# Performance work log

Measured on AMD Instinct MI355X. Metric: run time of the kernel, lower is better.

## Reference

```python
import jax, jax.numpy as jnp
from jax import lax
import numpy as np


def _conv(x, w):
    # x: [B,Cin,H,W], w: [Cout,Cin,kh,kw] -> [B,Cout,H,W], SAME padding
    return lax.conv_general_dilated(x, w, (1, 1), 'SAME')


def setup_inputs() -> dict:
    key = jax.random.key(0)
    ks = jax.random.split(key, 16)
    B, Hh, W = 8, 256, 256
    inputs = jax.random.normal(ks[0], (B, Hh, W), jnp.float32)
    H0 = jax.random.normal(ks[1], (B, Hh, W), jnp.float32)
    C0 = jax.random.normal(ks[2], (B, 2, Hh, W), jnp.float32)
    # learned scalars: c2 ~ U(0,1), sf ~ N(0, 0.01) shifted away from 0 (it is a divisor)
    c2 = jax.random.uniform(ks[3], (1,), jnp.float32, 0.0, 1.0)
    sf = 0.01 * jax.random.normal(ks[4], (1,), jnp.float32) + 0.02
    # RedNet (assumed small conv encoder-decoder): 1->32->64->32->1, 3x3 SAME, ReLU
    w1 = 0.1 * jax.random.normal(ks[5], (32, 1, 3, 3), jnp.float32)
    b1 = jnp.zeros((32,), jnp.float32)
    w2 = 0.1 * jax.random.normal(ks[6], (64, 32, 3, 3), jnp.float32)
    b2 = jnp.zeros((64,), jnp.float32)
    w3 = 0.1 * jax.random.normal(ks[7], (32, 64, 3, 3), jnp.float32)
    b3 = jnp.zeros((32,), jnp.float32)
    w4 = 0.1 * jax.random.normal(ks[8], (1, 32, 3, 3), jnp.float32)
    b4 = jnp.zeros((1,), jnp.float32)
    return dict(inputs=inputs, H0=H0, C0=C0, c2=c2, sf=sf,
                w1=w1, b1=b1, w2=w2, b2=b2, w3=w3, b3=b3, w4=w4, b4=b4)


def reference(inputs, H0, C0, c2, sf, w1, b1, w2, b2, w3, b3, w4, b4):
    # Fixed 5-point Laplacian stencil (non-trainable in the original module)
    lap_k = jnp.array([[0., 1., 0.], [1., -4., 1.], [0., 1., 0.]],
                      dtype=inputs.dtype)[None, None]  # [1,1,3,3]

    # torch chain: C' = permute/matmul(Wcc^T)/permute + wcu*U
    #   reduces exactly to: C'[:,0] = inputs, C'[:,1] = C_old[:,0]
    C_new = jnp.stack([inputs, C0[:, 0]], axis=1)  # [B,2,H,W]

    V = inputs - H0  # [B,H,W]

    # H = whc . C' = 2*C'[:,0] - C'[:,1] = 2*inputs - C_old[:,0]
    lap = _conv(inputs[:, None], lap_k)[:, 0]  # [B,H,W]
    H = 2.0 * inputs - C0[:, 0] + c2 * lap

    # RedNet on scaled residual V
    h = (V / sf)[:, None]  # [B,1,H,W]
    h = jax.nn.relu(_conv(h, w1) + b1[None, :, None, None])
    h = jax.nn.relu(_conv(h, w2) + b2[None, :, None, None])
    h = jax.nn.relu(_conv(h, w3) + b3[None, :, None, None])
    V_hat = (_conv(h, w4) + b4[None, :, None, None])[:, 0] * sf  # [B,H,W]

    outputs = H + V_hat
    return (outputs, H, C_new, V, V_hat)
```

## Files before the change

### kernel.cpp

```cpp
#include <hip/hip_runtime.h>

#define PLANE 65536
#define WIDTH 256
#define PADW 258
#define PADPLANE 66564

typedef __bf16 v8bf __attribute__((ext_vector_type(8)));
typedef float  v4f  __attribute__((ext_vector_type(4)));

typedef const __attribute__((address_space(1))) unsigned int* gas_ptr;
typedef __attribute__((address_space(3))) unsigned int* las_ptr;

__device__ __forceinline__ void gl_lds(const void* g, void* l) {
  __builtin_amdgcn_global_load_lds((gas_ptr)g, (las_ptr)l, 16, 0, 0);
}

__device__ __forceinline__ int swz(int c) {
  return (c & ~7) | ((c & 7) ^ ((c >> 3) & 7));
}

__device__ __forceinline__ unsigned int pack2(float a, float b) {
  __bf16 ba = (__bf16)a, bb = (__bf16)b;
  unsigned short sa = __builtin_bit_cast(unsigned short, ba);
  unsigned short sb = __builtin_bit_cast(unsigned short, bb);
  return (unsigned int)sa | ((unsigned int)sb << 16);
}

#define WT_N 37440
#define ZR_N (8 * 1028 * 64)
__global__ __launch_bounds__(256) void wz_k(
    const float* __restrict__ w1, const float* __restrict__ w2,
    const float* __restrict__ w3, const float* __restrict__ w4,
    float* __restrict__ w1t, __bf16* __restrict__ B2t,
    __bf16* __restrict__ B3t, float* __restrict__ w4t,
    __bf16* __restrict__ a1, __bf16* __restrict__ a2,
    __bf16* __restrict__ a3)
{
  int t = blockIdx.x * 256 + threadIdx.x;
  if (t < WT_N) {
    if (t < 288) {
      int tap = t >> 5, cout = t & 31;
      w1t[t] = w1[cout * 9 + tap];
    }
    int t2 = t - 288;
    if (t2 >= 0 && t2 < 18432) {
      int cout = t2 / 288, k = t2 % 288;
      int tap = k / 32, cin = k % 32;
      B2t[t2] = (__bf16)w2[cout * 288 + cin * 9 + tap];
    }
    int t3 = t - (288 + 18432);
    if (t3 >= 0 && t3 < 18432) {
      int cout = t3 / 576, k = t3 % 576;
      int tap = k / 64, cin = k % 64;
      B3t[t3] = (__bf16)w3[cout * 576 + cin * 9 + tap];
    }
    int t4 = t - (288 + 18432 + 18432);
    if (t4 >= 0 && t4 < 288) {
      int tap = t4 >> 5, cin = t4 & 31;
      w4t[t4] = w4[cin * 9 + tap];
    }
    return;
  }
  int idx = t - WT_N;
  if (idx >= ZR_N) return;
  unsigned int* p; int C2;
  const int R1 = 8 * 1028 * 16, R2 = 8 * 1028 * 32;
  if (idx < R1)           { p = (unsigned int*)a1; C2 = 16; }
  else if (idx < R1 + R2) { p = (unsigned int*)a2; C2 = 32; idx -= R1; }
  else                    { p = (unsigned int*)a3; C2 = 16; idx -= R1 + R2; }
  int ch = idx % C2;
  int pr = idx / C2;
  int b = pr / 1028, r = pr % 1028;
  int y, x;
  if      (r < 258) { y = 0;           x = r; }
  else if (r < 516) { y = 257;         x = r - 258; }
  else if (r < 772) { y = r - 516 + 1; x = 0; }
  else              { y = r - 772 + 1; x = 257; }
  p[((size_t)b * PADPLANE + y * PADW + x) * C2 + ch] = 0;
}

__global__ __launch_bounds__(256) void prepconv1_k(
    const float* __restrict__ inputs, const float* __restrict__ H0,
    const float* __restrict__ C0, const float* __restrict__ c2p,
    const float* __restrict__ sfp, const float* __restrict__ w1t,
    const float* __restrict__ b1, float* __restrict__ dout,
    __bf16* __restrict__ act1)
{
  const int x = threadIdx.x, y = blockIdx.x, b = blockIdx.y;
  const int p = b * PLANE + y * WIDTH + x;
  const float c2 = c2p[0], sf = sfp[0], rsf = 1.0f / sf;

  float iv[3][3], hv[3][3];
  #pragma unroll
  for (int dy = 0; dy < 3; dy++) {
    int yy = y + dy - 1;
    #pragma unroll
    for (int dx = 0; dx < 3; dx++) {
      int xx = x + dx - 1;
      bool ok = (yy >= 0 && yy < 256 && xx >= 0 && xx < 256);
      int pn = p + (dy - 1) * WIDTH + (dx - 1);
      iv[dy][dx] = ok ? inputs[pn] : 0.f;
      hv[dy][dx] = ok ? H0[pn]     : 0.f;
    }
  }
  const float in = iv[1][1], h0 = hv[1][1];
  const float c0a = C0[b * 131072 + y * WIDTH + x];
  float lap = iv[0][1] + iv[2][1] + iv[1][0] + iv[1][2] - 4.f * in;
  float Hv = 2.f * in - c0a + c2 * lap;
  float V  = in - h0;
  dout[524288 + p]  = Hv;
  dout[2097152 + p] = V;
  dout[1048576 + b * 131072 + y * WIDTH + x]         = in;
  dout[1048576 + b * 131072 + 65536 + y * WIDTH + x] = c0a;

  float acc[32];
  #pragma unroll
  for (int i = 0; i < 32; i++) acc[i] = b1[i];
  #pragma unroll
  for (int tap = 0; tap < 9; tap++) {
    float v = (iv[tap / 3][tap % 3] - hv[tap / 3][tap % 3]) * rsf;
    const float* wp = w1t + tap * 32;
    #pragma unroll
    for (int i = 0; i < 32; i++) acc[i] = fmaf(wp[i], v, acc[i]);
  }
  unsigned int u[16];
  #pragma unroll
  for (int j = 0; j < 16; j++)
    u[j] = pack2(fmaxf(acc[2*j], 0.f), fmaxf(acc[2*j+1], 0.f));
  size_t pa = ((size_t)b * PADPLANE + (y+1) * PADW + (x+1)) * 32;
  uint4* op = reinterpret_cast<uint4*>(act1 + pa);
  #pragma unroll
  for (int j = 0; j < 4; j++)
    op[j] = make_uint4(u[4*j], u[4*j+1], u[4*j+2], u[4*j+3]);
}

#define C2ROWB 8320
template<int ROWS>
__global__ __launch_bounds__(256, 2) void conv2_k(
    const __bf16* __restrict__ in, const __bf16* __restrict__ Bt,
    const float* __restrict__ bias, __bf16* __restrict__ out)
{
  const int lane = threadIdx.x & 63, wave = threadIdx.x >> 6;
  const int l15 = lane & 15, q = lane >> 4;
  const int y0 = blockIdx.x * ROWS, xt = blockIdx.y, b = blockIdx.z;
  const int x0 = xt * 128;
  __shared__ __align__(16) char smem[3 * C2ROWB];
  const __bf16* plane = in + (size_t)b * PADPLANE * 32;

  auto stage = [&](int pr, char* lrow) {
    const char* g = (const char*)(plane + ((size_t)pr * PADW + x0) * 32);
    const int base = wave * 130;
    #pragma unroll
    for (int j = 0; j < 2; j++) {
      int c = base + j * 64 + lane;
      gl_lds(g + (size_t)swz(c) * 16, lrow + (base + j * 64) * 16);
    }
    if (lane < 2) {
      int c = base + 128 + lane;
      gl_lds(g + (size_t)swz(c) * 16, lrow + (base + 128) * 16);
    }
  };

  v8bf breg[9][4];
  #pragma unroll
  for (int tap = 0; tap < 9; tap++)
    #pragma unroll
    for (int nt = 0; nt < 4; nt++)
      breg[tap][nt] = *(const v8bf*)(Bt + (size_t)(nt * 16 + l15) * 288
                                        + tap * 32 + q * 8);
  v4f bv[4];
  #pragma unroll
  for (int nt = 0; nt < 4; nt++) bv[nt] = *(const v4f*)(bias + nt * 16 + q * 4);

  #pragma unroll
  for (int r = 0; r < 3; r++) stage(y0 + r, smem + r * C2ROWB);
  __syncthreads();

  for (int i = 0; i < ROWS; i++) {
    v4f acc[2][4];
    #pragma unroll
    for (int mt = 0; mt < 2; mt++)
      #pragma unroll
      for (int nt = 0; nt < 4; nt++)
        acc[mt][nt] = bv[nt];

    #pragma unroll
    for (int tap = 0; tap < 9; tap++) {
      const int dy = tap / 3, dx = tap % 3;
      const char* srow = smem + ((i + dy) % 3) * C2ROWB;
      v8bf af[2];
      #pragma unroll
      for (int mt = 0; mt < 2; mt++) {
        int P = wave * 32 + mt * 16 + l15 + dx;
        af[mt] = *(const v8bf*)(srow + (size_t)swz(P * 4 + q) * 16);
      }
      #pragma unroll
      for (int mt = 0; mt < 2; mt++)
        #pragma unroll
        for (int nt = 0; nt < 4; nt++)
          acc[mt][nt] = __builtin_amdgcn_mfma_f32_16x16x32_bf16(
              breg[tap][nt], af[mt], acc[mt][nt], 0, 0, 0);
    }
    {
      size_t rb = ((size_t)b * PADPLANE + (size_t)(y0 + i + 1) * PADW
                   + x0 + 1) * 64;
      #pragma unroll
      for (int mt = 0; mt < 2; mt++) {
        size_t pa = rb + (size_t)(wave * 32 + mt * 16 + l15) * 64;
        #pragma unroll
        for (int nt = 0; nt < 4; nt++) {
          float r0 = fmaxf(acc[mt][nt][0], 0.f);
          float r1 = fmaxf(acc[mt][nt][1], 0.f);
          float r2 = fmaxf(acc[mt][nt][2], 0.f);
          float r3 = fmaxf(acc[mt][nt][3], 0.f);
          *(uint2*)(out + pa + nt * 16 + q * 4) =
              make_uint2(pack2(r0, r1), pack2(r2, r3));
        }
      }
    }
    __syncthreads();
    if (i + 3 < ROWS + 2)
      stage(y0 + i + 3, smem + (i % 3) * C2ROWB);
    __syncthreads();
  }
}

#define C3ROWB 16640
template<int ROWS>
__global__ __launch_bounds__(256, 2) void conv3_k(
    const __bf16* __restrict__ in, const __bf16* __restrict__ Bt,
    const float* __restrict__ bias, __bf16* __restrict__ out)
{
  const int lane = threadIdx.x & 63, wave = threadIdx.x >> 6;
  const int l15 = lane & 15, q = lane >> 4;
  const int y0 = blockIdx.x * ROWS, xt = blockIdx.y, b = blockIdx.z;
  const int x0 = xt * 128;
  __shared__ __align__(16) char smem[4 * C3ROWB];
  const __bf16* plane = in + (size_t)b * PADPLANE * 64;

  auto stage = [&](int pr, char* lrow) {
    const char* g = (const char*)(plane + ((size_t)pr * PADW + x0) * 64);
    const int base = wave * 260;
    #pragma unroll
    for (int j = 0; j < 4; j++) {
      int c = base + j * 64 + lane;
      gl_lds(g + (size_t)swz(c) * 16, lrow + (base + j * 64) * 16);
    }
    if (lane < 4) {
      int c = base + 256 + lane;
      gl_lds(g + (size_t)swz(c) * 16, lrow + (base + 256) * 16);
    }
  };

  v8bf breg[9][2][2];
  #pragma unroll
  for (int tap = 0; tap < 9; tap++)
    #pragma unroll
    for (int kb = 0; kb < 2; kb++)
      #pragma unroll
      for (int nt = 0; nt < 2; nt++)
        breg[tap][kb][nt] = *(const v8bf*)(Bt + (size_t)(nt * 16 + l15) * 576
                                              + tap * 64 + kb * 32 + q * 8);
  v4f bv[2];
  #pragma unroll
  for (int nt = 0; nt < 2; nt++) bv[nt] = *(const v4f*)(bias + nt * 16 + q * 4);

  #pragma unroll
  for (int r = 0; r < 4; r++) stage(y0 + r, smem + r * C3ROWB);
  __syncthreads();

  for (int ps = 0; ps < ROWS / 2; ps++) {
    v4f acc[2][2][2];
    #pragma unroll
    for (int rr = 0; rr < 2; rr++)
      #pragma unroll
      for (int mt = 0; mt < 2; mt++)
        #pragma unroll
        for (int nt = 0; nt < 2; nt++)
          acc[rr][mt][nt] = bv[nt];

    #pragma unroll
    for (int t = 0; t < 4; t++) {
      const char* srow = smem + ((2 * ps + t) & 3) * C3ROWB;
      #pragma unroll
      for (int dx = 0; dx < 3; dx++) {
        #pragma unroll
        for (int kb = 0; kb < 2; kb++) {
          v8bf af[2];
          #pragma unroll
          for (int mt = 0; mt < 2; mt++) {
            int P = wave * 32 + mt * 16 + l15 + dx;
            af[mt] = *(const v8bf*)(srow + (size_t)swz(P * 8 + kb * 4 + q) * 16);
          }
          #pragma unroll
          for (int mt = 0; mt < 2; mt++)
            #pragma unroll
            for (int nt = 0; nt < 2; nt++) {
              if (t <= 2)
                acc[0][mt][nt] = __builtin_amdgcn_mfma_f32_16x16x32_bf16(
                    breg[t * 3 + dx][kb][nt], af[mt], acc[0][mt][nt], 0, 0, 0);
              if (t >= 1)
                acc[1][mt][nt] = __builtin_amdgcn_mfma_f32_16x16x32_bf16(
                    breg[(t - 1) * 3 + dx][kb][nt], af[mt], acc[1][mt][nt],
                    0, 0, 0);
            }
        }
      }
    }
    #pragma unroll
    for (int rr = 0; rr < 2; rr++) {
      size_t rb = ((size_t)b * PADPLANE
                   + (size_t)(y0 + 2 * ps + rr + 1) * PADW + x0 + 1) * 32;
      #pragma unroll
      for (int mt = 0; mt < 2; mt++) {
        size_t pa = rb + (size_t)(wave * 32 + mt * 16 + l15) * 32;
        #pragma unroll
        for (int nt = 0; nt < 2; nt++) {
          float r0 = fmaxf(acc[rr][mt][nt][0], 0.f);
          float r1 = fmaxf(acc[rr][mt][nt][1], 0.f);
          float r2 = fmaxf(acc[rr][mt][nt][2], 0.f);
          float r3 = fmaxf(acc[rr][mt][nt][3], 0.f);
          *(uint2*)(out + pa + nt * 16 + q * 4) =
              make_uint2(pack2(r0, r1), pack2(r2, r3));
        }
      }
    }
    __syncthreads();
    if (ps + 1 < ROWS / 2) {
      stage(y0 + 2 * ps + 4, smem + ((2 * ps) & 3) * C3ROWB);
      stage(y0 + 2 * ps + 5, smem + ((2 * ps + 1) & 3) * C3ROWB);
    }
    __syncthreads();
  }
}

__global__ __launch_bounds__(256) void conv4_k(
    const __bf16* __restrict__ act3, const float* __restrict__ w4t,
    const float* __restrict__ b4, const float* __restrict__ sfp,
    float* __restrict__ dout)
{
  const int x = threadIdx.x, y0 = blockIdx.x * 2, b = blockIdx.y;
  const float b4v = b4[0], sf = sfp[0];
  const uint4* base = (const uint4*)(act3 + (size_t)b * PADPLANE * 32);
  float acc0 = b4v, acc1 = b4v;

  #pragma unroll
  for (int t = 0; t < 4; t++) {
    const uint4* rp = base + ((size_t)(y0 + t) * PADW + x) * 4;
    uint4 L[12];
    #pragma unroll
    for (int j = 0; j < 12; j++) L[j] = rp[j];
    #pragma unroll
    for (int j = 0; j < 12; j++) {
      const int dx = j >> 2, c0 = (j & 3) * 8;
      unsigned int uu[4] = {L[j].x, L[j].y, L[j].z, L[j].w};
      float f[8];
      #pragma unroll
      for (int k = 0; k < 4; k++) {
        f[2*k]   = __builtin_bit_cast(float, uu[k] << 16);
        f[2*k+1] = __builtin_bit_cast(float, uu[k] & 0xFFFF0000u);
      }
      if (t <= 2) {
        const float* wp = w4t + (t * 3 + dx) * 32 + c0;
        #pragma unroll
        for (int k = 0; k < 8; k++) acc0 = fmaf(wp[k], f[k], acc0);
      }
      if (t >= 1) {
        const float* wp = w4t + ((t - 1) * 3 + dx) * 32 + c0;
        #pragma unroll
        for (int k = 0; k < 8; k++) acc1 = fmaf(wp[k], f[k], acc1);
      }
    }
  }
  size_t p0 = ((size_t)b << 16) + (size_t)y0 * WIDTH + x;
  float vh0 = acc0 * sf, vh1 = acc1 * sf;
  dout[p0]                   = dout[524288 + p0] + vh0;
  dout[2621440 + p0]         = vh0;
  dout[p0 + WIDTH]           = dout[524288 + p0 + WIDTH] + vh1;
  dout[2621440 + p0 + WIDTH] = vh1;
}

extern "C" void kernel_launch(void* const* d_in, const int* in_sizes, int n_in,
                              void* d_out, int out_size, void* d_ws, size_t ws_size,
                              hipStream_t stream) {
  const float* inputs = (const float*)d_in[0];
  const float* H0     = (const float*)d_in[1];
  const float* C0     = (const float*)d_in[2];
  const float* c2     = (const float*)d_in[3];
  const float* sf     = (const float*)d_in[4];
  const float* w1     = (const float*)d_in[5];
  const float* b1     = (const float*)d_in[6];
  const float* w2     = (const float*)d_in[7];
  const float* b2     = (const float*)d_in[8];
  const float* w3     = (const float*)d_in[9];
  const float* b3     = (const float*)d_in[10];
  const float* w4     = (const float*)d_in[11];
  const float* b4     = (const float*)d_in[12];
  float* out = (float*)d_out;
  float* ws  = (float*)d_ws;

  float*  w1t  = ws;
  float*  w4t  = ws + 288;
  __bf16* B2t  = (__bf16*)(ws + 576);
  __bf16* B3t  = (__bf16*)(ws + 9792);
  __bf16* act1 = (__bf16*)(ws + 19008);
  __bf16* act2 = act1 + (size_t)8 * PADPLANE * 32;
  __bf16* act3 = act2 + (size_t)8 * PADPLANE * 64;

  wz_k<<<2203, 256, 0, stream>>>(w1, w2, w3, w4, w1t, B2t, B3t, w4t,
                                 act1, act2, act3);
  prepconv1_k<<<dim3(256, 8), 256, 0, stream>>>(inputs, H0, C0, c2, sf,
                                                w1t, b1, out, act1);
  conv2_k<8><<<dim3(32, 2, 8), 256, 0, stream>>>(act1, B2t, b2, act2);
  conv3_k<8><<<dim3(32, 2, 8), 256, 0, stream>>>(act2, B3t, b3, act3);
  conv4_k<<<dim3(128, 8), 256, 0, stream>>>(act3, w4t, b4, sf, out);
}
```

Baseline: 174.7 us.

## Prefetch next conv rows before compute and halve conv3 column tile

conv2 moves to a four-row LDS ring and issues the next row's async global-to-LDS load at the start of each iteration, so one barrier per row replaces two and the load overlaps the MFMA work. conv3 narrows its column tile from 128 to 64 pixels, doubling the grid to 512 blocks, and uses a six-row ring that prefetches the next two rows before computing the current pair. The intent is to hide global-load latency and raise occupancy and parallelism. In exchange each conv3 block does less compute per B-fragment register load, and relies on a single barrier to order ring-slot reuse.

After: 180.0 us. +3.0%, slower.

```diff
diff --git a/kernel.cpp b/kernel.cpp
--- a/kernel.cpp
+++ b/kernel.cpp
@@ -144,7 +144,7 @@
   const int l15 = lane & 15, q = lane >> 4;
   const int y0 = blockIdx.x * ROWS, xt = blockIdx.y, b = blockIdx.z;
   const int x0 = xt * 128;
-  __shared__ __align__(16) char smem[3 * C2ROWB];
+  __shared__ __align__(16) char smem[4 * C2ROWB];
   const __bf16* plane = in + (size_t)b * PADPLANE * 32;
 
   auto stage = [&](int pr, char* lrow) {
@@ -177,6 +177,9 @@
   __syncthreads();
 
   for (int i = 0; i < ROWS; i++) {
+    if (i + 3 < ROWS + 2)
+      stage(y0 + i + 3, smem + ((i + 3) & 3) * C2ROWB);
+
     v4f acc[2][4];
     #pragma unroll
     for (int mt = 0; mt < 2; mt++)
@@ -187,7 +190,7 @@
     #pragma unroll
     for (int tap = 0; tap < 9; tap++) {
       const int dy = tap / 3, dx = tap % 3;
-      const char* srow = smem + ((i + dy) % 3) * C2ROWB;
+      const char* srow = smem + ((i + dy) & 3) * C2ROWB;
       v8bf af[2];
       #pragma unroll
       for (int mt = 0; mt < 2; mt++) {
@@ -219,13 +222,10 @@
       }
     }
     __syncthreads();
-    if (i + 3 < ROWS + 2)
-      stage(y0 + i + 3, smem + (i % 3) * C2ROWB);
-    __syncthreads();
-  }
-}
-
-#define C3ROWB 16640
+  }
+}
+
+#define C3ROWB 8448
 template<int ROWS>
 __global__ __launch_bounds__(256, 2) void conv3_k(
     const __bf16* __restrict__ in, const __bf16* __restrict__ Bt,
@@ -234,21 +234,21 @@
   const int lane = threadIdx.x & 63, wave = threadIdx.x >> 6;
   const int l15 = lane & 15, q = lane >> 4;
   const int y0 = blockIdx.x * ROWS, xt = blockIdx.y, b = blockIdx.z;
-  const int x0 = xt * 128;
-  __shared__ __align__(16) char smem[4 * C3ROWB];
+  const int x0 = xt * 64;
+  __shared__ __align__(16) char smem[6 * C3ROWB];
   const __bf16* plane = in + (size_t)b * PADPLANE * 64;
 
   auto stage = [&](int pr, char* lrow) {
     const char* g = (const char*)(plane + ((size_t)pr * PADW + x0) * 64);
-    const int base = wave * 260;
-    #pragma unroll
-    for (int j = 0; j < 4; j++) {
+    const int base = wave * 132;
+    #pragma unroll
+    for (int j = 0; j < 2; j++) {
       int c = base + j * 64 + lane;
       gl_lds(g + (size_t)swz(c) * 16, lrow + (base + j * 64) * 16);
     }
     if (lane < 4) {
-      int c = base + 256 + lane;
-      gl_lds(g + (size_t)swz(c) * 16, lrow + (base + 256) * 16);
+      int c = base + 128 + lane;
+      gl_lds(g + (size_t)swz(c) * 16, lrow + (base + 128) * 16);
     }
   };
 
@@ -270,40 +270,36 @@
   __syncthreads();
 
   for (int ps = 0; ps < ROWS / 2; ps++) {
-    v4f acc[2][2][2];
+    if (2 * ps + 4 < ROWS + 2)
+      stage(y0 + 2 * ps + 4, smem + ((2 * ps + 4) % 6) * C3ROWB);
+    if (2 * ps + 5 < ROWS + 2)
+      stage(y0 + 2 * ps + 5, smem + ((2 * ps + 5) % 6) * C3ROWB);
+
+    v4f acc[2][2];
     #pragma unroll
     for (int rr = 0; rr < 2; rr++)
       #pragma unroll
-      for (int mt = 0; mt < 2; mt++)
-        #pragma unroll
-        for (int nt = 0; nt < 2; nt++)
-          acc[rr][mt][nt] = bv[nt];
+      for (int nt = 0; nt < 2; nt++)
+        acc[rr][nt] = bv[nt];
 
     #pragma unroll
     for (int t = 0; t < 4; t++) {
-      const char* srow = smem + ((2 * ps + t) & 3) * C3ROWB;
+      const char* srow = smem + ((2 * ps + t) % 6) * C3ROWB;
       #pragma unroll
       for (int dx = 0; dx < 3; dx++) {
         #pragma unroll
         for (int kb = 0; kb < 2; kb++) {
-          v8bf af[2];
+          int P = wave * 16 + l15 + dx;
+          v8bf af = *(const v8bf*)(srow + (size_t)swz(P * 8 + kb * 4 + q) * 16);
           #pragma unroll
-          for (int mt = 0; mt < 2; mt++) {
-            int P = wave * 32 + mt * 16 + l15 + dx;
-            af[mt] = *(const v8bf*)(srow + (size_t)swz(P * 8 + kb * 4 + q) * 16);
+          for (int nt = 0; nt < 2; nt++) {
+            if (t <= 2)
+              acc[0][nt] = __builtin_amdgcn_mfma_f32_16x16x32_bf16(
+                  breg[t * 3 + dx][kb][nt], af, acc[0][nt], 0, 0, 0);
+            if (t >= 1)
+              acc[1][nt] = __builtin_amdgcn_mfma_f32_16x16x32_bf16(
+                  breg[(t - 1) * 3 + dx][kb][nt], af, acc[1][nt], 0, 0, 0);
           }
-          #pragma unroll
-          for (int mt = 0; mt < 2; mt++)
-            #pragma unroll
-            for (int nt = 0; nt < 2; nt++) {
-              if (t <= 2)
-                acc[0][mt][nt] = __builtin_amdgcn_mfma_f32_16x16x32_bf16(
-                    breg[t * 3 + dx][kb][nt], af[mt], acc[0][mt][nt], 0, 0, 0);
-              if (t >= 1)
-                acc[1][mt][nt] = __builtin_amdgcn_mfma_f32_16x16x32_bf16(
-                    breg[(t - 1) * 3 + dx][kb][nt], af[mt], acc[1][mt][nt],
-                    0, 0, 0);
-            }
         }
       }
     }
@@ -311,24 +307,16 @@
     for (int rr = 0; rr < 2; rr++) {
       size_t rb = ((size_t)b * PADPLANE
                    + (size_t)(y0 + 2 * ps + rr + 1) * PADW + x0 + 1) * 32;
-      #pragma unroll
-      for (int mt = 0; mt < 2; mt++) {
-        size_t pa = rb + (size_t)(wave * 32 + mt * 16 + l15) * 32;
-        #pragma unroll
-        for (int nt = 0; nt < 2; nt++) {
-          float r0 = fmaxf(acc[rr][mt][nt][0], 0.f);
-          float r1 = fmaxf(acc[rr][mt][nt][1], 0.f);
-          float r2 = fmaxf(acc[rr][mt][nt][2], 0.f);
-          float r3 = fmaxf(acc[rr][mt][nt][3], 0.f);
-          *(uint2*)(out + pa + nt * 16 + q * 4) =
-              make_uint2(pack2(r0, r1), pack2(r2, r3));
-        }
-      }
-    }
-    __syncthreads();
-    if (ps + 1 < ROWS / 2) {
-      stage(y0 + 2 * ps + 4, smem + ((2 * ps) & 3) * C3ROWB);
-      stage(y0 + 2 * ps + 5, smem + ((2 * ps + 1) & 3) * C3ROWB);
+      size_t pa = rb + (size_t)(wave * 16 + l15) * 32;
+      #pragma unroll
+      for (int nt = 0; nt < 2; nt++) {
+        float r0 = fmaxf(acc[rr][nt][0], 0.f);
+        float r1 = fmaxf(acc[rr][nt][1], 0.f);
+        float r2 = fmaxf(acc[rr][nt][2], 0.f);
+        float r3 = fmaxf(acc[rr][nt][3], 0.f);
+        *(uint2*)(out + pa + nt * 16 + q * 4) =
+            make_uint2(pack2(r0, r1), pack2(r2, r3));
+      }
     }
     __syncthreads();
   }
@@ -412,6 +400,6 @@
   prepconv1_k<<<dim3(256, 8), 256, 0, stream>>>(inputs, H0, C0, c2, sf,
                                                 w1t, b1, out, act1);
   conv2_k<8><<<dim3(32, 2, 8), 256, 0, stream>>>(act1, B2t, b2, act2);
-  conv3_k<8><<<dim3(32, 2, 8), 256, 0, stream>>>(act2, B3t, b3, act3);
+  conv3_k<8><<<dim3(32, 4, 8), 256, 0, stream>>>(act2, B3t, b3, act3);
   conv4_k<<<dim3(128, 8), 256, 0, stream>>>(act3, w4t, b4, sf, out);
 }
```

## Prefetch next row in conv2, simplify conv3 to single-row ring, halve rows per block

Applied to the files above, without the earlier changes.

conv2 now uses a 4-slot LDS ring and issues the async load for the next input row before computing the current one, dropping one barrier per row so loads overlap MFMA work. conv3 drops its two-output-row register-reuse scheme and becomes a simple 3-slot, one-row-at-a-time loop using less LDS. Both kernels process 4 rows per block instead of 8, doubling the grid for more parallelism at the cost of more halo re-loading. The conv3 change gives up the reuse of A fragments across two output rows.

Measured after the change: 185.8 us. 6.3% more time.

```diff
diff --git a/kernel.cpp b/kernel.cpp
--- a/kernel.cpp
+++ b/kernel.cpp
@@ -144,7 +144,7 @@
   const int l15 = lane & 15, q = lane >> 4;
   const int y0 = blockIdx.x * ROWS, xt = blockIdx.y, b = blockIdx.z;
   const int x0 = xt * 128;
-  __shared__ __align__(16) char smem[3 * C2ROWB];
+  __shared__ __align__(16) char smem[4 * C2ROWB];
   const __bf16* plane = in + (size_t)b * PADPLANE * 32;
 
   auto stage = [&](int pr, char* lrow) {
@@ -177,6 +177,9 @@
   __syncthreads();
 
   for (int i = 0; i < ROWS; i++) {
+    if (i + 3 < ROWS + 2)
+      stage(y0 + i + 3, smem + ((i + 3) & 3) * C2ROWB);
+
     v4f acc[2][4];
     #pragma unroll
     for (int mt = 0; mt < 2; mt++)
@@ -187,7 +190,7 @@
     #pragma unroll
     for (int tap = 0; tap < 9; tap++) {
       const int dy = tap / 3, dx = tap % 3;
-      const char* srow = smem + ((i + dy) % 3) * C2ROWB;
+      const char* srow = smem + ((i + dy) & 3) * C2ROWB;
       v8bf af[2];
       #pragma unroll
       for (int mt = 0; mt < 2; mt++) {
@@ -218,9 +221,6 @@
         }
       }
     }
-    __syncthreads();
-    if (i + 3 < ROWS + 2)
-      stage(y0 + i + 3, smem + (i % 3) * C2ROWB);
     __syncthreads();
   }
 }
@@ -235,7 +235,7 @@
   const int l15 = lane & 15, q = lane >> 4;
   const int y0 = blockIdx.x * ROWS, xt = blockIdx.y, b = blockIdx.z;
   const int x0 = xt * 128;
-  __shared__ __align__(16) char smem[4 * C3ROWB];
+  __shared__ __align__(16) char smem[3 * C3ROWB];
   const __bf16* plane = in + (size_t)b * PADPLANE * 64;
 
   auto stage = [&](int pr, char* lrow) {
@@ -266,70 +266,57 @@
   for (int nt = 0; nt < 2; nt++) bv[nt] = *(const v4f*)(bias + nt * 16 + q * 4);
 
   #pragma unroll
-  for (int r = 0; r < 4; r++) stage(y0 + r, smem + r * C3ROWB);
+  for (int r = 0; r < 3; r++) stage(y0 + r, smem + r * C3ROWB);
   __syncthreads();
 
-  for (int ps = 0; ps < ROWS / 2; ps++) {
-    v4f acc[2][2][2];
-    #pragma unroll
-    for (int rr = 0; rr < 2; rr++)
-      #pragma unroll
-      for (int mt = 0; mt < 2; mt++)
-        #pragma unroll
-        for (int nt = 0; nt < 2; nt++)
-          acc[rr][mt][nt] = bv[nt];
-
-    #pragma unroll
-    for (int t = 0; t < 4; t++) {
-      const char* srow = smem + ((2 * ps + t) & 3) * C3ROWB;
-      #pragma unroll
-      for (int dx = 0; dx < 3; dx++) {
-        #pragma unroll
-        for (int kb = 0; kb < 2; kb++) {
-          v8bf af[2];
+  for (int i = 0; i < ROWS; i++) {
+    v4f acc[2][2];
+    #pragma unroll
+    for (int mt = 0; mt < 2; mt++)
+      #pragma unroll
+      for (int nt = 0; nt < 2; nt++)
+        acc[mt][nt] = bv[nt];
+
+    #pragma unroll
+    for (int tap = 0; tap < 9; tap++) {
+      const int dy = tap / 3, dx = tap % 3;
+      const char* srow = smem + ((i + dy) % 3) * C3ROWB;
+      #pragma unroll
+      for (int kb = 0; kb < 2; kb++) {
+        v8bf af[2];
+        #pragma unroll
+        for (int mt = 0; mt < 2; mt++) {
+          int P = wave * 32 + mt * 16 + l15 + dx;
+          af[mt] = *(const v8bf*)(srow + (size_t)swz(P * 8 + kb * 4 + q) * 16);
+        }
+        #pragma unroll
+        for (int mt = 0; mt < 2; mt++)
           #pragma unroll
-          for (int mt = 0; mt < 2; mt++) {
-            int P = wave * 32 + mt * 16 + l15 + dx;
-            af[mt] = *(const v8bf*)(srow + (size_t)swz(P * 8 + kb * 4 + q) * 16);
-          }
-          #pragma unroll
-          for (int mt = 0; mt < 2; mt++)
-            #pragma unroll
-            for (int nt = 0; nt < 2; nt++) {
-              if (t <= 2)
-                acc[0][mt][nt] = __builtin_amdgcn_mfma_f32_16x16x32_bf16(
-                    breg[t * 3 + dx][kb][nt], af[mt], acc[0][mt][nt], 0, 0, 0);
-              if (t >= 1)
-                acc[1][mt][nt] = __builtin_amdgcn_mfma_f32_16x16x32_bf16(
-                    breg[(t - 1) * 3 + dx][kb][nt], af[mt], acc[1][mt][nt],
-                    0, 0, 0);
-            }
-        }
-      }
-    }
-    #pragma unroll
-    for (int rr = 0; rr < 2; rr++) {
-      size_t rb = ((size_t)b * PADPLANE
-                   + (size_t)(y0 + 2 * ps + rr + 1) * PADW + x0 + 1) * 32;
+          for (int nt = 0; nt < 2; nt++)
+            acc[mt][nt] = __builtin_amdgcn_mfma_f32_16x16x32_bf16(
+                breg[tap][kb][nt], af[mt], acc[mt][nt], 0, 0, 0);
+      }
+    }
+    {
+      size_t rb = ((size_t)b * PADPLANE + (size_t)(y0 + i + 1) * PADW
+                   + x0 + 1) * 32;
       #pragma unroll
       for (int mt = 0; mt < 2; mt++) {
         size_t pa = rb + (size_t)(wave * 32 + mt * 16 + l15) * 32;
         #pragma unroll
         for (int nt = 0; nt < 2; nt++) {
-          float r0 = fmaxf(acc[rr][mt][nt][0], 0.f);
-          float r1 = fmaxf(acc[rr][mt][nt][1], 0.f);
-          float r2 = fmaxf(acc[rr][mt][nt][2], 0.f);
-          float r3 = fmaxf(acc[rr][mt][nt][3], 0.f);
+          float r0 = fmaxf(acc[mt][nt][0], 0.f);
+          float r1 = fmaxf(acc[mt][nt][1], 0.f);
+          float r2 = fmaxf(acc[mt][nt][2], 0.f);
+          float r3 = fmaxf(acc[mt][nt][3], 0.f);
           *(uint2*)(out + pa + nt * 16 + q * 4) =
               make_uint2(pack2(r0, r1), pack2(r2, r3));
         }
       }
     }
     __syncthreads();
-    if (ps + 1 < ROWS / 2) {
-      stage(y0 + 2 * ps + 4, smem + ((2 * ps) & 3) * C3ROWB);
-      stage(y0 + 2 * ps + 5, smem + ((2 * ps + 1) & 3) * C3ROWB);
-    }
+    if (i + 3 < ROWS + 2)
+      stage(y0 + i + 3, smem + (i % 3) * C3ROWB);
     __syncthreads();
   }
 }
@@ -411,7 +398,7 @@
                                  act1, act2, act3);
   prepconv1_k<<<dim3(256, 8), 256, 0, stream>>>(inputs, H0, C0, c2, sf,
                                                 w1t, b1, out, act1);
-  conv2_k<8><<<dim3(32, 2, 8), 256, 0, stream>>>(act1, B2t, b2, act2);
-  conv3_k<8><<<dim3(32, 2, 8), 256, 0, stream>>>(act2, B3t, b3, act3);
+  conv2_k<4><<<dim3(64, 2, 8), 256, 0, stream>>>(act1, B2t, b2, act2);
+  conv3_k<4><<<dim3(64, 2, 8), 256, 0, stream>>>(act2, B3t, b3, act3);
   conv4_k<<<dim3(128, 8), 256, 0, stream>>>(act3, w4t, b4, sf, out);
 }
```
